# Performance work log

Measured on AMD Instinct MI355X. Metric: run time of the kernel, lower is better.

The kernel has to match this reference:

```python
import jax, jax.numpy as jnp
import numpy as np

E = 8        # num_experts
K = 2        # num_experts_per_tok
H = 2048     # hidden_size
I = 1024     # intermediate_size (c_fc outputs 2*I for swiglu)
T = 4096     # tokens (batch*seq flattened)
STD = 0.02


def setup_inputs() -> dict:
    key = jax.random.key(0)
    k1, k2, k3, k4 = jax.random.split(key, 4)
    x = jax.random.normal(k1, (T, H), dtype=jnp.float32)
    router_w = jax.random.normal(k2, (E, H), dtype=jnp.float32) * STD   # nn.Linear(H->E, bias=False)
    w1 = jax.random.normal(k3, (E, 2 * I, H), dtype=jnp.float32) * STD  # c_fc.weight (E, out, in)
    w2 = jax.random.normal(k4, (E, H, I), dtype=jnp.float32) * STD      # c_proj.weight (E, out, in)
    return {"x": x, "router_w": router_w, "w1": w1, "w2": w2}


def reference(x, router_w, w1, w2):
    # Router: logits -> fp32 softmax -> top-k gates (no renorm), as in scattermoe-style MoE
    logits = x @ router_w.T                                   # (T, E)
    probs = jax.nn.softmax(logits.astype(jnp.float32), axis=-1)
    gates, expert_idx = jax.lax.top_k(probs, K)               # (T, K)

    # Grouped expert GEMMs, expressed densely over the small fixed expert axis.
    up = jnp.einsum('th,efh->etf', x, w1)                     # (E, T, 2I)  c_fc
    g = up[..., ::2]                                          # interleaved GLU gate
    u = up[..., 1::2]
    h = u * jax.nn.silu(g)                                    # swiglu, (E, T, I)
    y = jnp.einsum('eti,ehi->eth', h, w2)                     # (E, T, H)  c_proj

    # Scatter-combine: pick each token's top-k expert outputs, weight by gates.
    t = jnp.arange(T)[:, None]                                # (T, 1)
    sel = y[expert_idx, t]                                    # (T, K, H)
    out = jnp.sum(gates[..., None].astype(x.dtype) * sel, axis=1)  # (T, H)
    return out
```

## Files before the change

### kernel.cpp

```cpp
#include <hip/hip_runtime.h>
#include <hip/hip_bf16.h>
#include <stdint.h>

#define T_TOK 4096
#define H_DIM 2048
#define I_DIM 1024
#define E_NUM 8

using bf16x8  = __attribute__((ext_vector_type(8))) __bf16;
using f32x4   = __attribute__((ext_vector_type(4))) float;
using ushort8 = __attribute__((ext_vector_type(8))) unsigned short;

__device__ __forceinline__ unsigned short f2bf(float f) {
  unsigned int u = __float_as_uint(f);
  u += 0x7fffu + ((u >> 16) & 1u);
  return (unsigned short)(u >> 16);
}

__device__ __forceinline__ void gload16(const unsigned short* g, unsigned short* l) {
  __builtin_amdgcn_global_load_lds(
      (const __attribute__((address_space(1))) unsigned int*)(g),
      (__attribute__((address_space(3))) unsigned int*)(l), 16, 0, 0);
}

__global__ void k_cvt_w1(const float* __restrict__ w1, unsigned short* __restrict__ w1b) {
  size_t idx = (size_t)blockIdx.x * 256 + threadIdx.x;
  size_t d = idx * 8;
  int h = (int)(d & (size_t)(H_DIM - 1));
  size_t rem = d >> 11;
  int i = (int)(rem & (size_t)(I_DIM - 1));
  size_t rem2 = rem >> 10;
  int gu = (int)(rem2 & 1);
  int e = (int)(rem2 >> 1);
  const float* src = w1 + (((size_t)e * 2 * I_DIM + 2 * i + gu) * H_DIM + h);
  float4 v0 = *reinterpret_cast<const float4*>(src);
  float4 v1 = *reinterpret_cast<const float4*>(src + 4);
  ushort8 b;
  b[0] = f2bf(v0.x); b[1] = f2bf(v0.y); b[2] = f2bf(v0.z); b[3] = f2bf(v0.w);
  b[4] = f2bf(v1.x); b[5] = f2bf(v1.y); b[6] = f2bf(v1.z); b[7] = f2bf(v1.w);
  *reinterpret_cast<ushort8*>(w1b + d) = b;
}

__global__ void k_cvt_w2(const float* __restrict__ w2, unsigned short* __restrict__ w2b) {
  size_t d = ((size_t)blockIdx.x * 256 + threadIdx.x) * 8;
  float4 v0 = *reinterpret_cast<const float4*>(w2 + d);
  float4 v1 = *reinterpret_cast<const float4*>(w2 + d + 4);
  ushort8 b;
  b[0] = f2bf(v0.x); b[1] = f2bf(v0.y); b[2] = f2bf(v0.z); b[3] = f2bf(v0.w);
  b[4] = f2bf(v1.x); b[5] = f2bf(v1.y); b[6] = f2bf(v1.z); b[7] = f2bf(v1.w);
  *reinterpret_cast<ushort8*>(w2b + d) = b;
}

__global__ void k_router(const float* __restrict__ x, const float* __restrict__ rw,
                         float* __restrict__ gates, int* __restrict__ idxs,
                         unsigned int* __restrict__ counts, unsigned short* __restrict__ xb) {
  int t = blockIdx.x;
  int lane = threadIdx.x;
  float acc[E_NUM];
#pragma unroll
  for (int e = 0; e < E_NUM; e++) acc[e] = 0.f;
  const float* xrow = x + (size_t)t * H_DIM;
  for (int h = lane; h < H_DIM; h += 64) {
    float xv = xrow[h];
    xb[(size_t)t * H_DIM + h] = f2bf(xv);
#pragma unroll
    for (int e = 0; e < E_NUM; e++) acc[e] += xv * rw[e * H_DIM + h];
  }
#pragma unroll
  for (int e = 0; e < E_NUM; e++) {
#pragma unroll
    for (int off = 32; off >= 1; off >>= 1) acc[e] += __shfl_xor(acc[e], off, 64);
  }
  if (lane == 0) {
    float mx = acc[0];
#pragma unroll
    for (int e = 1; e < E_NUM; e++) mx = fmaxf(mx, acc[e]);
    float p[E_NUM], s = 0.f;
#pragma unroll
    for (int e = 0; e < E_NUM; e++) { p[e] = __expf(acc[e] - mx); s += p[e]; }
    float inv = 1.f / s;
#pragma unroll
    for (int e = 0; e < E_NUM; e++) p[e] *= inv;
    int i1 = 0, i2 = 0; float m1 = -1.f, m2 = -1.f;
#pragma unroll
    for (int e = 0; e < E_NUM; e++) {
      float v = p[e];
      if (v > m1)      { m2 = m1; i2 = i1; m1 = v; i1 = e; }
      else if (v > m2) { m2 = v; i2 = e; }
    }
    gates[t * 2 + 0] = m1; gates[t * 2 + 1] = m2;
    idxs[t * 2 + 0] = i1;  idxs[t * 2 + 1] = i2;
    atomicAdd(&counts[i1], 1u);
    atomicAdd(&counts[i2], 1u);
  }
}

__global__ void k_offsets(const unsigned int* __restrict__ counts,
                          unsigned int* __restrict__ off, unsigned int* __restrict__ cursor) {
  if (threadIdx.x == 0 && blockIdx.x == 0) {
    unsigned int o = 0;
    for (int e = 0; e < E_NUM; e++) { off[e] = o; cursor[e] = o; o += counts[e]; }
  }
}

__global__ void k_scatter(const float* __restrict__ gates, const int* __restrict__ idxs,
                          unsigned int* __restrict__ cursor,
                          int* __restrict__ rowlist, float* __restrict__ rowgate) {
  int t = blockIdx.x * blockDim.x + threadIdx.x;
  if (t >= T_TOK) return;
#pragma unroll
  for (int k = 0; k < 2; k++) {
    int e = idxs[t * 2 + k];
    unsigned int pos = atomicAdd(&cursor[e], 1u);
    rowlist[pos] = t;
    rowgate[pos] = gates[t * 2 + k];
  }
}

__launch_bounds__(256, 3)
__global__ void k_gemm1(const unsigned short* __restrict__ xb, const unsigned short* __restrict__ w1b,
                        const unsigned int* __restrict__ off, const unsigned int* __restrict__ counts,
                        const int* __restrict__ rowlist, unsigned short* __restrict__ hc) {
  int e = blockIdx.z;
  unsigned int cnt = counts[e];
  unsigned int rb = blockIdx.y;
  if (rb * 128u >= cnt) return;
  unsigned int o = off[e];
  int i0 = blockIdx.x * 64;

  __shared__ unsigned short a_lds[128 * 32];
  __shared__ unsigned short bg_lds[64 * 32];
  __shared__ unsigned short bu_lds[64 * 32];

  int tid = threadIdx.x, lane = tid & 63, wave = tid >> 6;
  int wr = wave >> 1, wc = wave & 1;

  const unsigned short* aptr[2];
  unsigned short* alds[2];
#pragma unroll
  for (int it = 0; it < 2; it++) {
    int flat = wave * 128 + it * 64 + lane;
    int row = flat >> 2, colq = flat & 3;
    unsigned int pos = rb * 128u + (unsigned int)row;
    unsigned int gp = o + (pos < cnt ? pos : cnt - 1u);
    int tok = rowlist[gp];
    aptr[it] = xb + (size_t)tok * H_DIM + colq * 8;
    alds[it] = &a_lds[(wave * 2 + it) * 512];
  }
  int flatB = wave * 64 + lane;
  int brow = flatB >> 2, bcolq = flatB & 3;
  const unsigned short* bptr_g = w1b + ((size_t)(e * 2 + 0) * I_DIM + i0 + brow) * H_DIM + bcolq * 8;
  const unsigned short* bptr_u = w1b + ((size_t)(e * 2 + 1) * I_DIM + i0 + brow) * H_DIM + bcolq * 8;
  unsigned short* blds_g = &bg_lds[wave * 512];
  unsigned short* blds_u = &bu_lds[wave * 512];

  f32x4 accg[4][2], accu[4][2];
#pragma unroll
  for (int m = 0; m < 4; m++)
#pragma unroll
    for (int n = 0; n < 2; n++) {
      accg[m][n] = f32x4{0.f, 0.f, 0.f, 0.f};
      accu[m][n] = f32x4{0.f, 0.f, 0.f, 0.f};
    }

  for (int k0 = 0; k0 < H_DIM; k0 += 32) {
    __syncthreads();
    gload16(aptr[0] + k0, alds[0]);
    gload16(aptr[1] + k0, alds[1]);
    gload16(bptr_g + k0, blds_g);
    gload16(bptr_u + k0, blds_u);
    __syncthreads();

    bf16x8 af[4], bgf[2], buf_[2];
#pragma unroll
    for (int m = 0; m < 4; m++) {
      int row = wr * 64 + m * 16 + (lane & 15);
      af[m] = *reinterpret_cast<const bf16x8*>(&a_lds[row * 32 + (lane >> 4) * 8]);
    }
#pragma unroll
    for (int n = 0; n < 2; n++) {
      int c = wc * 32 + n * 16 + (lane & 15);
      bgf[n]  = *reinterpret_cast<const bf16x8*>(&bg_lds[c * 32 + (lane >> 4) * 8]);
      buf_[n] = *reinterpret_cast<const bf16x8*>(&bu_lds[c * 32 + (lane >> 4) * 8]);
    }
#pragma unroll
    for (int m = 0; m < 4; m++)
#pragma unroll
      for (int n = 0; n < 2; n++) {
        accg[m][n] = __builtin_amdgcn_mfma_f32_16x16x32_bf16(af[m], bgf[n],  accg[m][n], 0, 0, 0);
        accu[m][n] = __builtin_amdgcn_mfma_f32_16x16x32_bf16(af[m], buf_[n], accu[m][n], 0, 0, 0);
      }
  }

#pragma unroll
  for (int m = 0; m < 4; m++)
#pragma unroll
    for (int n = 0; n < 2; n++)
#pragma unroll
      for (int r = 0; r < 4; r++) {
        unsigned int grow = rb * 128u + wr * 64 + m * 16 + (lane >> 4) * 4 + r;
        if (grow < cnt) {
          float g = accg[m][n][r], u = accu[m][n][r];
          float h = u * g / (1.f + __expf(-g));
          int ic = i0 + wc * 32 + n * 16 + (lane & 15);
          hc[(size_t)(o + grow) * I_DIM + ic] = f2bf(h);
        }
      }
}

__launch_bounds__(256, 3)
__global__ void k_gemm2(const unsigned short* __restrict__ hc, const unsigned short* __restrict__ w2b,
                        const unsigned int* __restrict__ off, const unsigned int* __restrict__ counts,
                        const int* __restrict__ rowlist, const float* __restrict__ rowgate,
                        float* __restrict__ out) {
  int e = blockIdx.z;
  unsigned int cnt = counts[e];
  unsigned int rb = blockIdx.y;
  if (rb * 128u >= cnt) return;
  unsigned int o = off[e];
  int h0 = blockIdx.x * 128;

  __shared__ unsigned short a_lds[128 * 32];
  __shared__ unsigned short b_lds[128 * 32];

  int tid = threadIdx.x, lane = tid & 63, wave = tid >> 6;
  int wr = wave >> 1, wc = wave & 1;

  const unsigned short* aptr[2];
  const unsigned short* bptr[2];
  unsigned short *alds[2], *blds[2];
#pragma unroll
  for (int it = 0; it < 2; it++) {
    int flat = wave * 128 + it * 64 + lane;
    int row = flat >> 2, colq = flat & 3;
    unsigned int pos = rb * 128u + (unsigned int)row;
    unsigned int posc = (pos < cnt ? pos : cnt - 1u);
    aptr[it] = hc + (size_t)(o + posc) * I_DIM + colq * 8;
    bptr[it] = w2b + ((size_t)e * H_DIM + h0 + row) * I_DIM + colq * 8;
    alds[it] = &a_lds[(wave * 2 + it) * 512];
    blds[it] = &b_lds[(wave * 2 + it) * 512];
  }

  f32x4 acc[4][4];
#pragma unroll
  for (int m = 0; m < 4; m++)
#pragma unroll
    for (int n = 0; n < 4; n++) acc[m][n] = f32x4{0.f, 0.f, 0.f, 0.f};

  for (int k0 = 0; k0 < I_DIM; k0 += 32) {
    __syncthreads();
    gload16(aptr[0] + k0, alds[0]);
    gload16(aptr[1] + k0, alds[1]);
    gload16(bptr[0] + k0, blds[0]);
    gload16(bptr[1] + k0, blds[1]);
    __syncthreads();

    bf16x8 af[4], bf[4];
#pragma unroll
    for (int m = 0; m < 4; m++) {
      int row = wr * 64 + m * 16 + (lane & 15);
      af[m] = *reinterpret_cast<const bf16x8*>(&a_lds[row * 32 + (lane >> 4) * 8]);
    }
#pragma unroll
    for (int n = 0; n < 4; n++) {
      int c = wc * 64 + n * 16 + (lane & 15);
      bf[n] = *reinterpret_cast<const bf16x8*>(&b_lds[c * 32 + (lane >> 4) * 8]);
    }
#pragma unroll
    for (int m = 0; m < 4; m++)
#pragma unroll
      for (int n = 0; n < 4; n++)
        acc[m][n] = __builtin_amdgcn_mfma_f32_16x16x32_bf16(af[m], bf[n], acc[m][n], 0, 0, 0);
  }

#pragma unroll
  for (int m = 0; m < 4; m++)
#pragma unroll
    for (int r = 0; r < 4; r++) {
      unsigned int grow = rb * 128u + wr * 64 + m * 16 + (lane >> 4) * 4 + r;
      if (grow < cnt) {
        int tok = rowlist[o + grow];
        float gate = rowgate[o + grow];
        float* orow = out + (size_t)tok * H_DIM + h0 + wc * 64;
#pragma unroll
        for (int n = 0; n < 4; n++) {
          atomicAdd(&orow[n * 16 + (lane & 15)], gate * acc[m][n][r]);
        }
      }
    }
}

extern "C" void kernel_launch(void* const* d_in, const int* in_sizes, int n_in,
                              void* d_out, int out_size, void* d_ws, size_t ws_size,
                              hipStream_t stream) {
  const float* x  = (const float*)d_in[0];
  const float* rw = (const float*)d_in[1];
  const float* w1 = (const float*)d_in[2];
  const float* w2 = (const float*)d_in[3];
  float* out = (float*)d_out;

  char* ws = (char*)d_ws;
  unsigned int* counts = (unsigned int*)(ws + 0);
  unsigned int* cursor = (unsigned int*)(ws + 64);
  unsigned int* off    = (unsigned int*)(ws + 128);
  float* gates   = (float*)(ws + 4096);
  int*   idxs    = (int*)(ws + 4096 + 32768);
  int*   rowlist = (int*)(ws + 4096 + 65536);
  float* rowgate = (float*)(ws + 4096 + 98304);
  unsigned short* xb  = (unsigned short*)(ws + (1ull << 20));
  unsigned short* hc  = (unsigned short*)(ws + (17ull << 20));
  unsigned short* w1b = (unsigned short*)(ws + (34ull << 20));
  unsigned short* w2b = (unsigned short*)(ws + (100ull << 20));

  hipMemsetAsync(ws, 0, 4096, stream);
  hipMemsetAsync(d_out, 0, (size_t)out_size * sizeof(float), stream);

  k_cvt_w1<<<(E_NUM * 2 * I_DIM * (H_DIM / 8) + 255) / 256, 256, 0, stream>>>(w1, w1b);
  k_cvt_w2<<<(E_NUM * H_DIM * (I_DIM / 8) + 255) / 256, 256, 0, stream>>>(w2, w2b);

  k_router<<<T_TOK, 64, 0, stream>>>(x, rw, gates, idxs, counts, xb);
  k_offsets<<<1, 64, 0, stream>>>(counts, off, cursor);
  k_scatter<<<T_TOK / 256, 256, 0, stream>>>(gates, idxs, cursor, rowlist, rowgate);
  k_gemm1<<<dim3(I_DIM / 64, T_TOK / 128, E_NUM), 256, 0, stream>>>(xb, w1b, off, counts, rowlist, hc);
  k_gemm2<<<dim3(H_DIM / 128, T_TOK / 128, E_NUM), 256, 0, stream>>>(hc, w2b, off, counts, rowlist, rowgate, out);
}
```

Measured before the change: 635.9 us.

## Double-buffer GEMM LDS with swizzle, widen gemm1 tile, replace atomics with combine

Both expert GEMMs now double-buffer LDS tiles so the next k-slice loads while the current one computes, with one barrier per step, and use an XOR swizzle on LDS rows to reduce bank conflicts. gemm1 widens its column tile to 128 and occupancy hint drops to 2. The down-projection writes gated per-slot rows into a workspace buffer (reusing the dead bf16 w1 region) and a new combine kernel sums each token's two slots, removing float atomics and the output memset. This adds an extra fp32 intermediate write/read pass and higher register pressure.

New measurement: 600.8 us. -5.5%, faster.

```diff
diff --git a/kernel.cpp b/kernel.cpp
--- a/kernel.cpp
+++ b/kernel.cpp
@@ -22,6 +22,8 @@
       (const __attribute__((address_space(1))) unsigned int*)(g),
       (__attribute__((address_space(3))) unsigned int*)(l), 16, 0, 0);
 }
+
+#define SWZ(row, qg) (((row) * 32) + ((((qg) ^ (((row) >> 1) & 3))) * 8))
 
 __global__ void k_cvt_w1(const float* __restrict__ w1, unsigned short* __restrict__ w1b) {
   size_t idx = (size_t)blockIdx.x * 256 + threadIdx.x;
@@ -105,7 +107,8 @@
 
 __global__ void k_scatter(const float* __restrict__ gates, const int* __restrict__ idxs,
                           unsigned int* __restrict__ cursor,
-                          int* __restrict__ rowlist, float* __restrict__ rowgate) {
+                          int* __restrict__ rowlist, float* __restrict__ rowgate,
+                          int* __restrict__ tok2slot) {
   int t = blockIdx.x * blockDim.x + threadIdx.x;
   if (t >= T_TOK) return;
 #pragma unroll
@@ -114,10 +117,11 @@
     unsigned int pos = atomicAdd(&cursor[e], 1u);
     rowlist[pos] = t;
     rowgate[pos] = gates[t * 2 + k];
-  }
-}
-
-__launch_bounds__(256, 3)
+    tok2slot[t * 2 + k] = (int)pos;
+  }
+}
+
+__launch_bounds__(256, 2)
 __global__ void k_gemm1(const unsigned short* __restrict__ xb, const unsigned short* __restrict__ w1b,
                         const unsigned int* __restrict__ off, const unsigned int* __restrict__ counts,
                         const int* __restrict__ rowlist, unsigned short* __restrict__ hc) {
@@ -126,93 +130,98 @@
   unsigned int rb = blockIdx.y;
   if (rb * 128u >= cnt) return;
   unsigned int o = off[e];
-  int i0 = blockIdx.x * 64;
-
-  __shared__ unsigned short a_lds[128 * 32];
-  __shared__ unsigned short bg_lds[64 * 32];
-  __shared__ unsigned short bu_lds[64 * 32];
+  int i0 = blockIdx.x * 128;
+
+  __shared__ unsigned short lds[2][12288];
 
   int tid = threadIdx.x, lane = tid & 63, wave = tid >> 6;
   int wr = wave >> 1, wc = wave & 1;
 
-  const unsigned short* aptr[2];
-  unsigned short* alds[2];
+  const unsigned short *aptr[2], *bgptr[2], *buptr[2];
 #pragma unroll
   for (int it = 0; it < 2; it++) {
-    int flat = wave * 128 + it * 64 + lane;
-    int row = flat >> 2, colq = flat & 3;
+    int flat = it * 256 + tid;
+    int row = flat >> 2, q = flat & 3;
+    int qs = q ^ ((row >> 1) & 3);
     unsigned int pos = rb * 128u + (unsigned int)row;
     unsigned int gp = o + (pos < cnt ? pos : cnt - 1u);
     int tok = rowlist[gp];
-    aptr[it] = xb + (size_t)tok * H_DIM + colq * 8;
-    alds[it] = &a_lds[(wave * 2 + it) * 512];
-  }
-  int flatB = wave * 64 + lane;
-  int brow = flatB >> 2, bcolq = flatB & 3;
-  const unsigned short* bptr_g = w1b + ((size_t)(e * 2 + 0) * I_DIM + i0 + brow) * H_DIM + bcolq * 8;
-  const unsigned short* bptr_u = w1b + ((size_t)(e * 2 + 1) * I_DIM + i0 + brow) * H_DIM + bcolq * 8;
-  unsigned short* blds_g = &bg_lds[wave * 512];
-  unsigned short* blds_u = &bu_lds[wave * 512];
-
-  f32x4 accg[4][2], accu[4][2];
+    aptr[it]  = xb + (size_t)tok * H_DIM + qs * 8;
+    bgptr[it] = w1b + ((size_t)(e * 2 + 0) * I_DIM + i0 + row) * H_DIM + qs * 8;
+    buptr[it] = w1b + ((size_t)(e * 2 + 1) * I_DIM + i0 + row) * H_DIM + qs * 8;
+  }
+
+  f32x4 accg[4][4], accu[4][4];
 #pragma unroll
   for (int m = 0; m < 4; m++)
 #pragma unroll
-    for (int n = 0; n < 2; n++) {
+    for (int n = 0; n < 4; n++) {
       accg[m][n] = f32x4{0.f, 0.f, 0.f, 0.f};
       accu[m][n] = f32x4{0.f, 0.f, 0.f, 0.f};
     }
 
-  for (int k0 = 0; k0 < H_DIM; k0 += 32) {
+#pragma unroll
+  for (int it = 0; it < 2; it++) {
+    gload16(aptr[it],  &lds[0][(it * 256 + tid) * 8]);
+    gload16(bgptr[it], &lds[0][4096 + (it * 256 + tid) * 8]);
+    gload16(buptr[it], &lds[0][8192 + (it * 256 + tid) * 8]);
+  }
+
+  int cur = 0;
+  int qg = lane >> 4;
+  for (int step = 0; step < H_DIM / 32; ++step) {
     __syncthreads();
-    gload16(aptr[0] + k0, alds[0]);
-    gload16(aptr[1] + k0, alds[1]);
-    gload16(bptr_g + k0, blds_g);
-    gload16(bptr_u + k0, blds_u);
-    __syncthreads();
-
-    bf16x8 af[4], bgf[2], buf_[2];
+    if (step + 1 < H_DIM / 32) {
+      int k0 = (step + 1) * 32;
+#pragma unroll
+      for (int it = 0; it < 2; it++) {
+        gload16(aptr[it] + k0,  &lds[cur ^ 1][(it * 256 + tid) * 8]);
+        gload16(bgptr[it] + k0, &lds[cur ^ 1][4096 + (it * 256 + tid) * 8]);
+        gload16(buptr[it] + k0, &lds[cur ^ 1][8192 + (it * 256 + tid) * 8]);
+      }
+    }
+    bf16x8 af[4], bgf[4], buf_[4];
 #pragma unroll
     for (int m = 0; m < 4; m++) {
       int row = wr * 64 + m * 16 + (lane & 15);
-      af[m] = *reinterpret_cast<const bf16x8*>(&a_lds[row * 32 + (lane >> 4) * 8]);
-    }
-#pragma unroll
-    for (int n = 0; n < 2; n++) {
-      int c = wc * 32 + n * 16 + (lane & 15);
-      bgf[n]  = *reinterpret_cast<const bf16x8*>(&bg_lds[c * 32 + (lane >> 4) * 8]);
-      buf_[n] = *reinterpret_cast<const bf16x8*>(&bu_lds[c * 32 + (lane >> 4) * 8]);
+      af[m] = *reinterpret_cast<const bf16x8*>(&lds[cur][SWZ(row, qg)]);
+    }
+#pragma unroll
+    for (int n = 0; n < 4; n++) {
+      int c = wc * 64 + n * 16 + (lane & 15);
+      bgf[n]  = *reinterpret_cast<const bf16x8*>(&lds[cur][4096 + SWZ(c, qg)]);
+      buf_[n] = *reinterpret_cast<const bf16x8*>(&lds[cur][8192 + SWZ(c, qg)]);
     }
 #pragma unroll
     for (int m = 0; m < 4; m++)
 #pragma unroll
-      for (int n = 0; n < 2; n++) {
+      for (int n = 0; n < 4; n++) {
         accg[m][n] = __builtin_amdgcn_mfma_f32_16x16x32_bf16(af[m], bgf[n],  accg[m][n], 0, 0, 0);
         accu[m][n] = __builtin_amdgcn_mfma_f32_16x16x32_bf16(af[m], buf_[n], accu[m][n], 0, 0, 0);
       }
+    cur ^= 1;
   }
 
 #pragma unroll
   for (int m = 0; m < 4; m++)
 #pragma unroll
-    for (int n = 0; n < 2; n++)
+    for (int n = 0; n < 4; n++)
 #pragma unroll
       for (int r = 0; r < 4; r++) {
         unsigned int grow = rb * 128u + wr * 64 + m * 16 + (lane >> 4) * 4 + r;
         if (grow < cnt) {
           float g = accg[m][n][r], u = accu[m][n][r];
           float h = u * g / (1.f + __expf(-g));
-          int ic = i0 + wc * 32 + n * 16 + (lane & 15);
+          int ic = i0 + wc * 64 + n * 16 + (lane & 15);
           hc[(size_t)(o + grow) * I_DIM + ic] = f2bf(h);
         }
       }
 }
 
-__launch_bounds__(256, 3)
+__launch_bounds__(256, 2)
 __global__ void k_gemm2(const unsigned short* __restrict__ hc, const unsigned short* __restrict__ w2b,
                         const unsigned int* __restrict__ off, const unsigned int* __restrict__ counts,
-                        const int* __restrict__ rowlist, const float* __restrict__ rowgate,
-                        float* __restrict__ out) {
+                        const float* __restrict__ rowgate, float* __restrict__ y) {
   int e = blockIdx.z;
   unsigned int cnt = counts[e];
   unsigned int rb = blockIdx.y;
@@ -220,25 +229,21 @@
   unsigned int o = off[e];
   int h0 = blockIdx.x * 128;
 
-  __shared__ unsigned short a_lds[128 * 32];
-  __shared__ unsigned short b_lds[128 * 32];
+  __shared__ unsigned short lds[2][8192];
 
   int tid = threadIdx.x, lane = tid & 63, wave = tid >> 6;
   int wr = wave >> 1, wc = wave & 1;
 
-  const unsigned short* aptr[2];
-  const unsigned short* bptr[2];
-  unsigned short *alds[2], *blds[2];
+  const unsigned short *aptr[2], *bptr[2];
 #pragma unroll
   for (int it = 0; it < 2; it++) {
-    int flat = wave * 128 + it * 64 + lane;
-    int row = flat >> 2, colq = flat & 3;
+    int flat = it * 256 + tid;
+    int row = flat >> 2, q = flat & 3;
+    int qs = q ^ ((row >> 1) & 3);
     unsigned int pos = rb * 128u + (unsigned int)row;
     unsigned int posc = (pos < cnt ? pos : cnt - 1u);
-    aptr[it] = hc + (size_t)(o + posc) * I_DIM + colq * 8;
-    bptr[it] = w2b + ((size_t)e * H_DIM + h0 + row) * I_DIM + colq * 8;
-    alds[it] = &a_lds[(wave * 2 + it) * 512];
-    blds[it] = &b_lds[(wave * 2 + it) * 512];
+    aptr[it] = hc + (size_t)(o + posc) * I_DIM + qs * 8;
+    bptr[it] = w2b + ((size_t)e * H_DIM + h0 + row) * I_DIM + qs * 8;
   }
 
   f32x4 acc[4][4];
@@ -247,30 +252,41 @@
 #pragma unroll
     for (int n = 0; n < 4; n++) acc[m][n] = f32x4{0.f, 0.f, 0.f, 0.f};
 
-  for (int k0 = 0; k0 < I_DIM; k0 += 32) {
+#pragma unroll
+  for (int it = 0; it < 2; it++) {
+    gload16(aptr[it], &lds[0][(it * 256 + tid) * 8]);
+    gload16(bptr[it], &lds[0][4096 + (it * 256 + tid) * 8]);
+  }
+
+  int cur = 0;
+  int qg = lane >> 4;
+  for (int step = 0; step < I_DIM / 32; ++step) {
     __syncthreads();
-    gload16(aptr[0] + k0, alds[0]);
-    gload16(aptr[1] + k0, alds[1]);
-    gload16(bptr[0] + k0, blds[0]);
-    gload16(bptr[1] + k0, blds[1]);
-    __syncthreads();
-
+    if (step + 1 < I_DIM / 32) {
+      int k0 = (step + 1) * 32;
+#pragma unroll
+      for (int it = 0; it < 2; it++) {
+        gload16(aptr[it] + k0, &lds[cur ^ 1][(it * 256 + tid) * 8]);
+        gload16(bptr[it] + k0, &lds[cur ^ 1][4096 + (it * 256 + tid) * 8]);
+      }
+    }
     bf16x8 af[4], bf[4];
 #pragma unroll
     for (int m = 0; m < 4; m++) {
       int row = wr * 64 + m * 16 + (lane & 15);
-      af[m] = *reinterpret_cast<const bf16x8*>(&a_lds[row * 32 + (lane >> 4) * 8]);
+      af[m] = *reinterpret_cast<const bf16x8*>(&lds[cur][SWZ(row, qg)]);
     }
 #pragma unroll
     for (int n = 0; n < 4; n++) {
       int c = wc * 64 + n * 16 + (lane & 15);
-      bf[n] = *reinterpret_cast<const bf16x8*>(&b_lds[c * 32 + (lane >> 4) * 8]);
+      bf[n] = *reinterpret_cast<const bf16x8*>(&lds[cur][4096 + SWZ(c, qg)]);
     }
 #pragma unroll
     for (int m = 0; m < 4; m++)
 #pragma unroll
       for (int n = 0; n < 4; n++)
         acc[m][n] = __builtin_amdgcn_mfma_f32_16x16x32_bf16(af[m], bf[n], acc[m][n], 0, 0, 0);
+    cur ^= 1;
   }
 
 #pragma unroll
@@ -279,15 +295,29 @@
     for (int r = 0; r < 4; r++) {
       unsigned int grow = rb * 128u + wr * 64 + m * 16 + (lane >> 4) * 4 + r;
       if (grow < cnt) {
-        int tok = rowlist[o + grow];
         float gate = rowgate[o + grow];
-        float* orow = out + (size_t)tok * H_DIM + h0 + wc * 64;
-#pragma unroll
-        for (int n = 0; n < 4; n++) {
-          atomicAdd(&orow[n * 16 + (lane & 15)], gate * acc[m][n][r]);
-        }
-      }
-    }
+        float* yrow = y + (size_t)(o + grow) * H_DIM + h0 + wc * 64;
+#pragma unroll
+        for (int n = 0; n < 4; n++) yrow[n * 16 + (lane & 15)] = gate * acc[m][n][r];
+      }
+    }
+}
+
+__global__ void k_combine(const float* __restrict__ y, const int* __restrict__ tok2slot,
+                          float* __restrict__ out) {
+  int t = blockIdx.x * 4 + (threadIdx.x >> 6);
+  int lane = threadIdx.x & 63;
+  const float* y1 = y + (size_t)tok2slot[t * 2 + 0] * H_DIM;
+  const float* y2 = y + (size_t)tok2slot[t * 2 + 1] * H_DIM;
+  float* orow = out + (size_t)t * H_DIM;
+#pragma unroll
+  for (int h = 0; h < H_DIM; h += 256) {
+    int idx = h + lane * 4;
+    float4 a = *reinterpret_cast<const float4*>(&y1[idx]);
+    float4 b = *reinterpret_cast<const float4*>(&y2[idx]);
+    float4 rsum{a.x + b.x, a.y + b.y, a.z + b.z, a.w + b.w};
+    *reinterpret_cast<float4*>(&orow[idx]) = rsum;
+  }
 }
 
 extern "C" void kernel_launch(void* const* d_in, const int* in_sizes, int n_in,
@@ -303,24 +333,26 @@
   unsigned int* counts = (unsigned int*)(ws + 0);
   unsigned int* cursor = (unsigned int*)(ws + 64);
   unsigned int* off    = (unsigned int*)(ws + 128);
-  float* gates   = (float*)(ws + 4096);
-  int*   idxs    = (int*)(ws + 4096 + 32768);
-  int*   rowlist = (int*)(ws + 4096 + 65536);
-  float* rowgate = (float*)(ws + 4096 + 98304);
+  float* gates    = (float*)(ws + 4096);
+  int*   idxs     = (int*)(ws + 4096 + 32768);
+  int*   rowlist  = (int*)(ws + 4096 + 65536);
+  float* rowgate  = (float*)(ws + 4096 + 98304);
+  int*   tok2slot = (int*)(ws + 4096 + 131072);
   unsigned short* xb  = (unsigned short*)(ws + (1ull << 20));
   unsigned short* hc  = (unsigned short*)(ws + (17ull << 20));
   unsigned short* w1b = (unsigned short*)(ws + (34ull << 20));
   unsigned short* w2b = (unsigned short*)(ws + (100ull << 20));
+  float* y = (float*)(ws + (34ull << 20));
 
   hipMemsetAsync(ws, 0, 4096, stream);
-  hipMemsetAsync(d_out, 0, (size_t)out_size * sizeof(float), stream);
 
   k_cvt_w1<<<(E_NUM * 2 * I_DIM * (H_DIM / 8) + 255) / 256, 256, 0, stream>>>(w1, w1b);
   k_cvt_w2<<<(E_NUM * H_DIM * (I_DIM / 8) + 255) / 256, 256, 0, stream>>>(w2, w2b);
 
   k_router<<<T_TOK, 64, 0, stream>>>(x, rw, gates, idxs, counts, xb);
   k_offsets<<<1, 64, 0, stream>>>(counts, off, cursor);
-  k_scatter<<<T_TOK / 256, 256, 0, stream>>>(gates, idxs, cursor, rowlist, rowgate);
-  k_gemm1<<<dim3(I_DIM / 64, T_TOK / 128, E_NUM), 256, 0, stream>>>(xb, w1b, off, counts, rowlist, hc);
-  k_gemm2<<<dim3(H_DIM / 128, T_TOK / 128, E_NUM), 256, 0, stream>>>(hc, w2b, off, counts, rowlist, rowgate, out);
-}
+  k_scatter<<<T_TOK / 256, 256, 0, stream>>>(gates, idxs, cursor, rowlist, rowgate, tok2slot);
+  k_gemm1<<<dim3(I_DIM / 128, T_TOK / 128, E_NUM), 256, 0, stream>>>(xb, w1b, off, counts, rowlist, hc);
+  k_gemm2<<<dim3(H_DIM / 128, T_TOK / 128, E_NUM), 256, 0, stream>>>(hc, w2b, off, counts, rowgate, y);
+  k_combine<<<T_TOK / 4, 256, 0, stream>>>(y, tok2slot, out);
+}
```
